# Kernel optimization log

Hardware: AMD Instinct MI355X
Metric: run time of the kernel (lower is better)

## Reference

```python
import jax, jax.numpy as jnp
import numpy as np

B, T, D, H, K = 128, 64, 2048, 512, 512
WINDOWS = [2, 3, 4]
ROUT = 2 * H            # bidirectional GRU output dim = 1024
FIN = ROUT + len(WINDOWS) * K + 2048 + 1024  # 5632 ('full' concat)
FOUT = 2048
BN_EPS = 1e-5


def setup_inputs() -> dict:
    key = jax.random.key(0)
    ks = jax.random.split(key, 32)
    s = 0.02
    inp = {
        "videos": jax.random.normal(ks[0], (B, T, D), jnp.float32),
        "motions": jax.random.normal(ks[1], (B, 1024), jnp.float32),
        "videos_origin": jax.random.normal(ks[2], (B, 2048), jnp.float32),
        "lengths": jax.random.randint(ks[3], (B,), 1, T + 1, jnp.int32),
        # GRU params (PyTorch layout: gates ordered r,z,n stacked on dim 0)
        "Wih_f": jax.random.normal(ks[4], (3 * H, D), jnp.float32) * s,
        "Whh_f": jax.random.normal(ks[5], (3 * H, H), jnp.float32) * s,
        "bih_f": jnp.zeros((3 * H,), jnp.float32),
        "bhh_f": jnp.zeros((3 * H,), jnp.float32),
        "Wih_b": jax.random.normal(ks[6], (3 * H, D), jnp.float32) * s,
        "Whh_b": jax.random.normal(ks[7], (3 * H, H), jnp.float32) * s,
        "bih_b": jnp.zeros((3 * H,), jnp.float32),
        "bhh_b": jnp.zeros((3 * H,), jnp.float32),
        # FC + BatchNorm1d (eval-mode) of MFC
        "fc_w": jax.random.normal(ks[8], (FOUT, FIN), jnp.float32) * (np.sqrt(6.0) / np.sqrt(FIN + FOUT)),
        "fc_b": jnp.zeros((FOUT,), jnp.float32),
        "bn_gamma": jnp.ones((FOUT,), jnp.float32),
        "bn_beta": jnp.zeros((FOUT,), jnp.float32),
        "bn_mean": jnp.zeros((FOUT,), jnp.float32),
        "bn_var": jnp.ones((FOUT,), jnp.float32),
    }
    for i, ws in enumerate(WINDOWS):
        inp[f"conv_w{ws}"] = jax.random.normal(ks[10 + 2 * i], (K, 1, ws, ROUT), jnp.float32) * s
        inp[f"conv_b{ws}"] = jnp.zeros((K,), jnp.float32)
    # mask consistent with lengths: mask[b,t] = t < lengths[b]
    inp["videos_mask"] = (jnp.arange(T)[None, :] < inp["lengths"][:, None]).astype(jnp.float32)
    return inp


def _gru_dir(x, Wih, Whh, bih, bhh, reverse):
    # x: [B,T,D] -> outputs [B,T,H]; torch GRU cell with r,z,n gate order
    xg = jnp.einsum("btd,gd->btg", x, Wih) + bih  # [B,T,3H] precomputed input gates

    def step(h, xg_t):
        hg = h @ Whh.T + bhh
        xr, xz, xn = jnp.split(xg_t, 3, axis=-1)
        hr, hz, hn = jnp.split(hg, 3, axis=-1)
        r = jax.nn.sigmoid(xr + hr)
        z = jax.nn.sigmoid(xz + hz)
        n = jnp.tanh(xn + r * hn)
        h_new = (1.0 - z) * n + z * h
        return h_new, h_new

    h0 = jnp.zeros((x.shape[0], Whh.shape[1]), x.dtype)
    _, hs = jax.lax.scan(step, h0, jnp.swapaxes(xg, 0, 1), reverse=reverse)
    return jnp.swapaxes(hs, 0, 1)


def _conv_branch(x4, w, b, ws):
    # x4: [B,1,T,ROUT], w: [K,1,ws,ROUT]; torch padding=(ws-1, 0)
    y = jax.lax.conv_general_dilated(
        x4, w, (1, 1), [(ws - 1, ws - 1), (0, 0)],
        dimension_numbers=("NCHW", "OIHW", "NCHW"))  # [B,K,T+ws-1,1]
    y = jax.nn.relu(y + b[None, :, None, None])
    return jnp.max(y, axis=(2, 3))  # max_pool1d over full time -> [B,K]


def _forward(videos, motions, videos_origin, lengths, videos_mask,
             Wih_f, Whh_f, bih_f, bhh_f, Wih_b, Whh_b, bih_b, bhh_b,
             conv_w2, conv_b2, conv_w3, conv_b3, conv_w4, conv_b4,
             fc_w, fc_b, bn_gamma, bn_beta, bn_mean, bn_var):
    fwd = _gru_dir(videos, Wih_f, Whh_f, bih_f, bhh_f, reverse=False)
    bwd = _gru_dir(videos, Wih_b, Whh_b, bih_b, bhh_b, reverse=True)
    gru_init_out = jnp.concatenate([fwd, bwd], axis=-1)  # [B,T,2H]

    # masked mean over valid frames (vectorized version of the batch for-loop)
    denom = lengths.astype(gru_init_out.dtype)[:, None]
    gru_out = jnp.sum(gru_init_out * videos_mask[:, :, None], axis=1) / denom  # [B,2H]

    masked = gru_init_out * videos_mask[:, :, None]
    x4 = masked[:, None, :, :]  # [B,1,T,2H]
    con_out = jnp.concatenate([
        _conv_branch(x4, conv_w2, conv_b2, 2),
        _conv_branch(x4, conv_w3, conv_b3, 3),
        _conv_branch(x4, conv_w4, conv_b4, 4),
    ], axis=1)  # [B,3K]

    # concate == 'full' (dropout is identity in eval)
    features = jnp.concatenate([gru_out, con_out, videos_origin, motions], axis=1)
    features = features @ fc_w.T + fc_b
    # BatchNorm1d, eval mode with running stats
    features = bn_gamma * (features - bn_mean) * jax.lax.rsqrt(bn_var + BN_EPS) + bn_beta
    # l2norm over dim 1
    features = features / jnp.sqrt(jnp.sum(features * features, axis=1, keepdims=True))
    return features


def reference(videos, motions, videos_origin, lengths, videos_mask,
              Wih_f, Whh_f, bih_f, bhh_f, Wih_b, Whh_b, bih_b, bhh_b,
              conv_w2, conv_b2, conv_w3, conv_b3, conv_w4, conv_b4,
              fc_w, fc_b, bn_gamma, bn_beta, bn_mean, bn_var):
    return _forward(videos, motions, videos_origin, lengths, videos_mask,
                    Wih_f, Whh_f, bih_f, bhh_f, Wih_b, Whh_b, bih_b, bhh_b,
                    conv_w2, conv_b2, conv_w3, conv_b3, conv_w4, conv_b4,
                    fc_w, fc_b, bn_gamma, bn_beta, bn_mean, bn_var)
```

## Files before the change

kernel.cpp:

```cpp
#include <hip/hip_runtime.h>
#include <hip/hip_bf16.h>
#include <stdint.h>

typedef __attribute__((ext_vector_type(8))) short short8;
typedef __attribute__((ext_vector_type(4))) float floatx4;
typedef __attribute__((ext_vector_type(4))) unsigned int u32x4;
typedef unsigned short u16;
typedef unsigned int u32;
typedef unsigned long long u64;

static __device__ __forceinline__ u16 f2bf(float f) {
  union { float f; u32 u; } v; v.f = f;
  return (u16)((v.u + 0x7fffu + ((v.u >> 16) & 1u)) >> 16);
}
static __device__ __forceinline__ float bf2f(u16 h) {
  union { u32 u; float f; } v; v.u = ((u32)h) << 16; return v.f;
}
static __device__ __forceinline__ u64 pack4(float a, float b, float c, float d) {
  return (u64)f2bf(a) | ((u64)f2bf(b) << 16) | ((u64)f2bf(c) << 32) | ((u64)f2bf(d) << 48);
}

__global__ __launch_bounds__(256) void k_fused_cvt(
    const float* __restrict__ videos, const float* __restrict__ Wih_f,
    const float* __restrict__ Wih_b, const float* __restrict__ Whh_f,
    const float* __restrict__ Whh_b, const float* __restrict__ fc_w,
    const float* __restrict__ w2, const float* __restrict__ w3,
    const float* __restrict__ w4, const float* __restrict__ vo,
    const float* __restrict__ mo, const float* __restrict__ bih_f,
    const float* __restrict__ bih_b, const float* __restrict__ fcb,
    const float* __restrict__ gam, const float* __restrict__ bet,
    const float* __restrict__ mu, const float* __restrict__ var,
    u16* __restrict__ vid, u16* __restrict__ wih, u16* __restrict__ whh,
    u16* __restrict__ fcw, u16* __restrict__ wc, u16* __restrict__ feat,
    float* __restrict__ bihcat, float* __restrict__ bns, float* __restrict__ bnt)
{
  const int O1 = 4194304;
  const int O2 = O1 + 786432;
  const int O3 = O2 + 786432;
  const int O4 = O3 + 196608;
  const int O5 = O4 + 196608;
  const int O6 = O5 + 2883584;
  const int O7 = O6 + 1179648;
  const int O8 = O7 + 65536;
  const int O9 = O8 + 32768;
  const int NQ = O9 + 1280;
  for (int q = blockIdx.x * 256 + threadIdx.x; q < NQ; q += gridDim.x * 256) {
    if (q < O1) {
      float4 v = ((const float4*)videos)[q];
      ((u64*)vid)[q] = pack4(v.x, v.y, v.z, v.w);
    } else if (q < O2) {
      int r = q - O1; float4 v = ((const float4*)Wih_f)[r];
      ((u64*)wih)[r] = pack4(v.x, v.y, v.z, v.w);
    } else if (q < O3) {
      int r = q - O2; float4 v = ((const float4*)Wih_b)[r];
      ((u64*)wih)[r + 786432] = pack4(v.x, v.y, v.z, v.w);
    } else if (q < O4) {
      int r = q - O3; float4 v = ((const float4*)Whh_f)[r];
      ((u64*)whh)[r] = pack4(v.x, v.y, v.z, v.w);
    } else if (q < O5) {
      int r = q - O4; float4 v = ((const float4*)Whh_b)[r];
      ((u64*)whh)[r + 196608] = pack4(v.x, v.y, v.z, v.w);
    } else if (q < O6) {
      int r = q - O5; float4 v = ((const float4*)fc_w)[r];
      ((u64*)fcw)[r] = pack4(v.x, v.y, v.z, v.w);
    } else if (q < O7) {
      int r = q - O6;
      int e = r << 2;
      int row = e >> 10, col = e & 1023;
      const float* src;
      if (row < 1024)      { int j = row >> 9, k = row & 511;                 src = w2 + (k * 2 + j) * 1024; }
      else if (row < 2560) { int m = row - 1024; int j = m >> 9, k = m & 511; src = w3 + (k * 3 + j) * 1024; }
      else                 { int m = row - 2560; int j = m >> 9, k = m & 511; src = w4 + (k * 4 + j) * 1024; }
      float4 v = *(const float4*)(src + col);
      ((u64*)wc)[r] = pack4(v.x, v.y, v.z, v.w);
    } else if (q < O8) {
      int r = q - O7; int b = r >> 9, c = (r & 511) * 4;
      float4 v = *(const float4*)&vo[(long)b * 2048 + c];
      *(u64*)&feat[(long)b * 5632 + 2560 + c] = pack4(v.x, v.y, v.z, v.w);
    } else if (q < O9) {
      int r = q - O8; int b = r >> 8, c = (r & 255) * 4;
      float4 v = *(const float4*)&mo[(long)b * 1024 + c];
      *(u64*)&feat[(long)b * 5632 + 4608 + c] = pack4(v.x, v.y, v.z, v.w);
    } else {
      int r = q - O9;
      if (r < 768) {
        int i = r * 4;
        const float* s = (i < 1536) ? (bih_f + i) : (bih_b + (i - 1536));
        *(float4*)&bihcat[i] = *(const float4*)s;
      } else {
        int i = (r - 768) * 4;
#pragma unroll
        for (int j = 0; j < 4; ++j) {
          int idx = i + j;
          float sc = gam[idx] * rsqrtf(var[idx] + 1e-5f);
          bns[idx] = sc;
          bnt[idx] = sc * (fcb[idx] - mu[idx]) + bet[idx];
        }
      }
    }
  }
}

static __device__ __forceinline__ void gload_lds16(const u16* g, u16* l) {
  __builtin_amdgcn_global_load_lds((const __attribute__((address_space(1))) u32*)(const void*)g,
                                   (__attribute__((address_space(3))) u32*)(void*)l, 16, 0, 0);
}

__global__ __launch_bounds__(256) void gemm_bt(
    const u16* __restrict__ A, const u16* __restrict__ Bm,
    float* __restrict__ C, u16* __restrict__ C16, int M, int N, int K, int kn,
    const float* __restrict__ scale, const float* __restrict__ shift)
{
  __shared__ u16 As[128 * 32];
  __shared__ u16 Bs[128 * 32];
  int tid = threadIdx.x, lane = tid & 63, wid = tid >> 6;
  int nwg = gridDim.x * gridDim.y;
  int lin = blockIdx.y * gridDim.x + blockIdx.x;
  int q8 = nwg >> 3;
  int swz = (lin & 7) * q8 + (lin >> 3);
  int m0 = (swz / gridDim.x) * 128, n0 = (swz % gridDim.x) * 128;
  int kt0 = blockIdx.z * kn;
  int wr = wid >> 1, wc = wid & 1;
  int r16 = lane & 15, kq = lane >> 4;
  const floatx4 z4 = {0.f, 0.f, 0.f, 0.f};
  floatx4 acc[4][4];
#pragma unroll
  for (int i = 0; i < 4; ++i)
#pragma unroll
    for (int j = 0; j < 4; ++j) acc[i][j] = z4;
  for (int kt = kt0; kt < kt0 + kn; ++kt) {
    __syncthreads();
#pragma unroll
    for (int inst = 0; inst < 2; ++inst) {
      int g = inst * 256 + tid;
      int row = g >> 2, cb = g & 3;
      const u16* ga = A + (long)(m0 + row) * K + kt * 32 + cb * 8;
      const u16* gb = Bm + (long)(n0 + row) * K + kt * 32 + cb * 8;
      gload_lds16(ga, &As[(inst * 256 + wid * 64) * 8]);
      gload_lds16(gb, &Bs[(inst * 256 + wid * 64) * 8]);
    }
    __syncthreads();
    short8 af[4], bf[4];
#pragma unroll
    for (int mt = 0; mt < 4; ++mt) af[mt] = *(const short8*)&As[(wr * 64 + mt * 16 + r16) * 32 + kq * 8];
#pragma unroll
    for (int nt = 0; nt < 4; ++nt) bf[nt] = *(const short8*)&Bs[(wc * 64 + nt * 16 + r16) * 32 + kq * 8];
#pragma unroll
    for (int mt = 0; mt < 4; ++mt)
#pragma unroll
      for (int nt = 0; nt < 4; ++nt)
        acc[mt][nt] = __builtin_amdgcn_mfma_f32_16x16x32_bf16(af[mt], bf[nt], acc[mt][nt], 0, 0, 0);
  }
  float* Cp = C + (long)blockIdx.z * M * N;
#pragma unroll
  for (int nt = 0; nt < 4; ++nt) {
    int col = n0 + wc * 64 + nt * 16 + r16;
    float sc = scale ? scale[col] : 1.f;
    float sh = shift ? shift[col] : 0.f;
#pragma unroll
    for (int mt = 0; mt < 4; ++mt)
#pragma unroll
      for (int q = 0; q < 4; ++q) {
        int row = m0 + wr * 64 + mt * 16 + kq * 4 + q;
        float v = acc[mt][nt][q] * sc + sh;
        if (C16) C16[(long)row * N + col] = f2bf(v);
        else     Cp[(long)row * N + col] = v;
      }
  }
}

__global__ __launch_bounds__(512) void gru_rec(
    const float* __restrict__ xg,
    const u16* __restrict__ whhb,
    const float* __restrict__ bhh_f, const float* __restrict__ bhh_b,
    u16* __restrict__ hbuf,
    u16* __restrict__ maskb,
    u16* __restrict__ feat,
    const int* __restrict__ lengths,
    int* __restrict__ flg)
{
  __shared__ float part[2][4][3][256];
  __shared__ u16 hstage[8192];
  int tid = threadIdx.x, lane = tid & 63, wid = tid >> 6;
  int bid = blockIdx.x;
  int dir = bid >> 6, rem = bid & 63, bt = rem >> 3, is = rem & 7;
  int ih = wid & 3, ks = wid >> 2;
  int gbase = (dir * 8 + bt) * 32;
  int r16 = lane & 15, kq = lane >> 4;
  int iglob = is * 64 + ih * 16 + r16;
  int i0 = is * 64 + ih * 16 + kq * 4;
  int batch = bt * 16 + r16;
  int pollidx = (gbase + (lane & 31)) * 16;
  int pubidx = (gbase + is * 4 + ih) * 16;
  const float* bhh = dir ? bhh_b : bhh_f;
  const floatx4 z4 = {0.f, 0.f, 0.f, 0.f};
  int len = lengths[batch];

  short8 wfrag[3][8];
#pragma unroll
  for (int g = 0; g < 3; ++g) {
    const u16* wrow = whhb + (long)(dir * 1536 + g * 512 + iglob) * 512;
#pragma unroll
    for (int kk = 0; kk < 8; ++kk)
      wfrag[g][kk] = *(const short8*)&wrow[(ks * 8 + kk) * 32 + kq * 8];
  }
  float4 bh4[3];
#pragma unroll
  for (int g = 0; g < 3; ++g) bh4[g] = *(const float4*)&bhh[g * 512 + i0];
  float4 hprev = {0.f, 0.f, 0.f, 0.f};
  float4 msum = {0.f, 0.f, 0.f, 0.f};

  float4 px[3];
  if (ks == 0) {
    int ts0 = dir ? 63 : 0;
    long xb = (long)(batch * 64 + ts0) * 3072 + dir * 1536 + i0;
#pragma unroll
    for (int g = 0; g < 3; ++g) px[g] = *(const float4*)&xg[xb + g * 512];
  }

  int so0 = wid * 2048 + lane * 16;
  int so1 = so0 + 1024;
  char* sl0 = (char*)hstage + (so0 ^ (((so0 >> 10) & 7) << 4));
  char* sl1 = (char*)hstage + (so1 ^ (((so1 >> 10) & 7) << 4));
  int rb = r16 * 1024 + ks * 512 + kq * 16;
  int rsw = (r16 & 7) << 4;

  for (int t = 0; t < 64; ++t) {
    if (t > 0) {
      if (wid == 0) {
        while (true) {
          int v;
          asm volatile("global_load_dword %0, %1, off sc0 sc1\n\ts_waitcnt vmcnt(0)"
                       : "=v"(v) : "v"(&flg[pollidx]) : "memory");
          if (__all(v >= t)) break;
          __builtin_amdgcn_s_sleep(1);
        }
      }
      asm volatile("s_barrier" ::: "memory");
    }
    int par = t & 1;
    const char* hsrc = (const char*)(hbuf + (long)((par * 2 + dir) * 128 + bt * 16) * 512);
    u32x4 qa, qb;
    asm volatile(
      "global_load_dwordx4 %0, %2, off sc0 sc1\n\t"
      "global_load_dwordx4 %1, %3, off sc0 sc1"
      : "=&v"(qa), "=&v"(qb)
      : "v"(hsrc + so0), "v"(hsrc + so1)
      : "memory");
    asm volatile("s_waitcnt vmcnt(0)" ::: "memory");
    *(u32x4*)sl0 = qa;
    *(u32x4*)sl1 = qb;
    float4 pxn[3];
    if (ks == 0 && t < 63) {
      int ts1 = dir ? (62 - t) : (t + 1);
      long xb = (long)(batch * 64 + ts1) * 3072 + dir * 1536 + i0;
#pragma unroll
      for (int g = 0; g < 3; ++g) pxn[g] = *(const float4*)&xg[xb + g * 512];
    }
    asm volatile("s_waitcnt lgkmcnt(0)\n\ts_barrier" ::: "memory");
    floatx4 acc[3];
#pragma unroll
    for (int g = 0; g < 3; ++g) acc[g] = z4;
#pragma unroll
    for (int kk = 0; kk < 8; ++kk) {
      short8 hv = *(const short8*)((const char*)hstage + ((rb + kk * 64) ^ rsw));
#pragma unroll
      for (int g = 0; g < 3; ++g)
        acc[g] = __builtin_amdgcn_mfma_f32_16x16x32_bf16(wfrag[g][kk], hv, acc[g], 0, 0, 0);
    }
    if (ks == 1) {
#pragma unroll
      for (int g = 0; g < 3; ++g) *(floatx4*)&part[par][ih][g][lane * 4] = acc[g];
    }
    asm volatile("s_waitcnt lgkmcnt(0)\n\ts_barrier" ::: "memory");
    if (ks == 0) {
      int tsrc = dir ? (63 - t) : t;
#pragma unroll
      for (int g = 0; g < 3; ++g) acc[g] += *(const floatx4*)&part[par][ih][g][lane * 4];
      float4 hn4;
#pragma unroll
      for (int q = 0; q < 4; ++q) {
        float rr = acc[0][q] + ((const float*)&bh4[0])[q] + ((const float*)&px[0])[q];
        float zz = acc[1][q] + ((const float*)&bh4[1])[q] + ((const float*)&px[1])[q];
        float r = 1.f / (1.f + __expf(-rr));
        float z = 1.f / (1.f + __expf(-zz));
        float n = tanhf(((const float*)&px[2])[q] + r * (acc[2][q] + ((const float*)&bh4[2])[q]));
        ((float*)&hn4)[q] = (1.f - z) * n + z * ((const float*)&hprev)[q];
      }
      hprev = hn4;
      u16* hdst = hbuf + (long)(((par ^ 1) * 2 + dir) * 128 + bt * 16) * 512;
      u64 hval = pack4(hn4.x, hn4.y, hn4.z, hn4.w);
      asm volatile("global_store_dwordx2 %0, %1, off sc0 sc1"
                   :: "v"((u64*)&hdst[r16 * 512 + i0]), "v"(hval) : "memory");
      if (t < 63) {
        asm volatile("s_waitcnt vmcnt(0)" ::: "memory");
        if (lane == 0) {
          int tv = t + 1;
          asm volatile("global_store_dword %0, %1, off sc0 sc1"
                       :: "v"(&flg[pubidx]), "v"(tv) : "memory");
        }
      }
      bool mv = tsrc < len;
      *(u64*)&maskb[(long)(batch * 64 + tsrc) * 1024 + dir * 512 + i0] = mv ? hval : 0ull;
      if (mv) {
        msum.x += hn4.x; msum.y += hn4.y; msum.z += hn4.z; msum.w += hn4.w;
      }
      px[0] = pxn[0]; px[1] = pxn[1]; px[2] = pxn[2];
    }
  }
  if (ks == 0) {
    float inv = 1.0f / (float)len;
    *(u64*)&feat[(long)batch * 5632 + dir * 512 + i0] =
        pack4(msum.x * inv, msum.y * inv, msum.z * inv, msum.w * inv);
  }
}

__global__ __launch_bounds__(256) void k_conv_finish(
    const u16* __restrict__ z, const float* __restrict__ cb2,
    const float* __restrict__ cb3, const float* __restrict__ cb4,
    u16* __restrict__ feat)
{
  int b = blockIdx.x, wsi = blockIdx.y, k2 = threadIdx.x * 2;
  int ws = wsi + 2;
  int base = (wsi == 0) ? 0 : (wsi == 1 ? 1024 : 2560);
  const float* cb = (wsi == 0) ? cb2 : (wsi == 1 ? cb3 : cb4);
  float bias0 = cb[k2], bias1 = cb[k2 + 1];
  float m0 = 0.f, m1 = 0.f;
  for (int p = 0; p < 64 + ws - 1; ++p) {
    float a0 = bias0, a1 = bias1;
    for (int j = 0; j < ws; ++j) {
      int t = p - (ws - 1) + j;
      if (t >= 0 && t < 64) {
        u32 v = *(const u32*)&z[(long)(b * 64 + t) * 4608 + base + j * 512 + k2];
        a0 += bf2f((u16)v);
        a1 += bf2f((u16)(v >> 16));
      }
    }
    m0 = fmaxf(m0, a0);
    m1 = fmaxf(m1, a1);
  }
  *(u32*)&feat[(long)b * 5632 + 1024 + wsi * 512 + k2] = (u32)f2bf(m0) | ((u32)f2bf(m1) << 16);
}

__global__ __launch_bounds__(256) void k_l2norm(const float* __restrict__ p,
    const float* __restrict__ bns, const float* __restrict__ bnt, float* __restrict__ out)
{
  __shared__ float red[4];
  int b = blockIdx.x, tid = threadIdx.x;
  float v[8]; float s = 0.f;
#pragma unroll
  for (int j = 0; j < 8; ++j) {
    int i = j * 256 + tid;
    long o = (long)b * 2048 + i;
    float a = 0.f;
#pragma unroll
    for (int zz = 0; zz < 8; ++zz) a += p[o + (long)zz * 262144];
    a = a * bns[i] + bnt[i];
    v[j] = a; s += a * a;
  }
#pragma unroll
  for (int o = 32; o > 0; o >>= 1) s += __shfl_down(s, o);
  if ((tid & 63) == 0) red[tid >> 6] = s;
  __syncthreads();
  float rn = rsqrtf(red[0] + red[1] + red[2] + red[3]);
#pragma unroll
  for (int j = 0; j < 8; ++j)
    out[(long)b * 2048 + j * 256 + tid] = v[j] * rn;
}

extern "C" void kernel_launch(void* const* d_in, const int* in_sizes, int n_in,
                              void* d_out, int out_size, void* d_ws, size_t ws_size,
                              hipStream_t stream)
{
  (void)in_sizes; (void)n_in; (void)out_size; (void)ws_size;
  const float* videos       = (const float*)d_in[0];
  const float* motions      = (const float*)d_in[1];
  const float* videos_origin= (const float*)d_in[2];
  const int*   lengths      = (const int*)d_in[3];
  const float* Wih_f = (const float*)d_in[4];
  const float* Whh_f = (const float*)d_in[5];
  const float* bih_f = (const float*)d_in[6];
  const float* bhh_f = (const float*)d_in[7];
  const float* Wih_b = (const float*)d_in[8];
  const float* Whh_b = (const float*)d_in[9];
  const float* bih_b = (const float*)d_in[10];
  const float* bhh_b = (const float*)d_in[11];
  const float* fc_w  = (const float*)d_in[12];
  const float* fc_b  = (const float*)d_in[13];
  const float* bn_gamma = (const float*)d_in[14];
  const float* bn_beta  = (const float*)d_in[15];
  const float* bn_mean  = (const float*)d_in[16];
  const float* bn_var   = (const float*)d_in[17];
  const float* conv_w2 = (const float*)d_in[18];
  const float* conv_b2 = (const float*)d_in[19];
  const float* conv_w3 = (const float*)d_in[20];
  const float* conv_b3 = (const float*)d_in[21];
  const float* conv_w4 = (const float*)d_in[22];
  const float* conv_b4 = (const float*)d_in[23];
  float* out = (float*)d_out;
  char* w = (char*)d_ws;

  const size_t XG    = 0;
  const size_t HS    = 100663296;
  const size_t VID   = 134217728;
  const size_t MASKB = 167772160;
  const size_t WIH   = 184549376;
  const size_t WHH   = 197132288;
  const size_t WC    = 200278016;
  const size_t FCW   = 209715200;
  const size_t FEAT  = 232783872;
  const size_t BIH   = 235274240;
  const size_t BNS   = 235286528;
  const size_t BNT   = 235294720;
  const size_t HB    = 235302912;
  const size_t FLG   = HB + 524288;
  (void)HS;

  float* xg   = (float*)(w + XG);
  u16*   zb16 = (u16*)(w + XG);
  u16* vid    = (u16*)(w + VID);
  u16* maskb  = (u16*)(w + MASKB);
  float* fcp  = (float*)(w + MASKB);
  u16* wih    = (u16*)(w + WIH);
  u16* whh    = (u16*)(w + WHH);
  u16* wc_    = (u16*)(w + WC);
  u16* fcw    = (u16*)(w + FCW);
  u16* feat   = (u16*)(w + FEAT);
  float* bih  = (float*)(w + BIH);
  float* bns  = (float*)(w + BNS);
  float* bnt  = (float*)(w + BNT);
  u16* hb     = (u16*)(w + HB);
  int* flg    = (int*)(w + FLG);

  hipMemsetAsync(w + HB, 0, 524288 + 32768, stream);

  k_fused_cvt<<<4096, 256, 0, stream>>>(
      videos, Wih_f, Wih_b, Whh_f, Whh_b, fc_w, conv_w2, conv_w3, conv_w4,
      videos_origin, motions, bih_f, bih_b, fc_b, bn_gamma, bn_beta, bn_mean, bn_var,
      vid, wih, whh, fcw, wc_, feat, bih, bns, bnt);

  gemm_bt<<<dim3(24, 64), 256, 0, stream>>>(vid, wih, xg, nullptr, 8192, 3072, 2048, 64, nullptr, bih);

  {
    const float* xg_c = xg; const u16* whh_c = whh;
    u16* hb_c = hb; u16* mb_c = maskb; u16* ft_c = feat;
    const int* len_c = lengths; int* flg_c = flg;
    const float* bf_c = bhh_f; const float* bb_c = bhh_b;
    void* args[] = { (void*)&xg_c, (void*)&whh_c, (void*)&bf_c, (void*)&bb_c,
                     (void*)&hb_c, (void*)&mb_c, (void*)&ft_c, (void*)&len_c, (void*)&flg_c };
    hipLaunchCooperativeKernel(reinterpret_cast<void*>(gru_rec), dim3(128), dim3(512), args, 0, stream);
  }

  gemm_bt<<<dim3(36, 64), 256, 0, stream>>>(maskb, wc_, nullptr, zb16, 8192, 4608, 1024, 32, nullptr, nullptr);
  k_conv_finish<<<dim3(128, 3), 256, 0, stream>>>(zb16, conv_b2, conv_b3, conv_b4, feat);
  gemm_bt<<<dim3(16, 1, 8), 256, 0, stream>>>(feat, fcw, fcp, nullptr, 128, 2048, 5632, 22, nullptr, nullptr);
  k_l2norm<<<128, 256, 0, stream>>>(fcp, bns, bnt, out);
}
```

Measured before the change: 641.6 us.

## Add 256x256-tile pipelined GEMM kernel for input-gate and conv GEMMs

Adds a new 512-thread GEMM kernel that uses 256x256 output tiles with 64-wide K tiles, double-buffered LDS loaded through global_load_lds, an XOR-swizzled LDS layout, and MFMA clusters interleaved with the staging of the next tile's halves under raised wave priority. The GRU input-gate GEMM and the conv-window GEMM switch from the 128x128 gemm_bt to this kernel. The aim is more operand reuse per LDS load and better overlap of global loads with MFMA work on these large GEMMs. In exchange it uses 128KB of LDS and many accumulators per wave, which limits occupancy, and its wrap-around prefetch indexing is intricate.

```diff
diff --git a/kernel.cpp b/kernel.cpp
--- a/kernel.cpp
+++ b/kernel.cpp
@@ -106,6 +106,154 @@
                                    (__attribute__((address_space(3))) u32*)(void*)l, 16, 0, 0);
 }
 
+static __device__ __forceinline__ void stage_half_256(
+    const u16* __restrict__ Mat, long K, int rowbase, int ktile, u16* lregion,
+    int tid, int wid)
+{
+  int srow = tid >> 3;
+  int sce = (((tid >> 3) ^ tid) & 7) * 8;
+  const u16* g0 = Mat + (long)(rowbase + srow) * K + ktile * 64 + sce;
+  const u16* g1 = Mat + (long)(rowbase + 64 + srow) * K + ktile * 64 + sce;
+  gload_lds16(g0, lregion + wid * 512);
+  gload_lds16(g1, lregion + 4096 + wid * 512);
+}
+
+__global__ __launch_bounds__(512) void gemm256(
+    const u16* __restrict__ A, const u16* __restrict__ Bm,
+    float* __restrict__ C, u16* __restrict__ C16, int M, int N, int K, int NT,
+    const float* __restrict__ shift)
+{
+  __shared__ u16 lds[65536];
+  int tid = threadIdx.x, lane = tid & 63, wid = tid >> 6;
+  int r16 = lane & 15, kq = lane >> 4;
+  int wr = wid >> 2, wc = wid & 3;
+  int nwg = gridDim.x * gridDim.y;
+  int lin = blockIdx.y * gridDim.x + blockIdx.x;
+  int q8 = nwg >> 3;
+  int swz = (lin & 7) * q8 + (lin >> 3);
+  int m0 = (swz / gridDim.x) * 256, n0 = (swz % gridDim.x) * 256;
+
+  int fxor = (r16 & 7) << 4;
+  int c0 = (kq * 16) ^ fxor;
+  int c1 = c0 ^ 64;
+  int brow0 = (wc & 1) * 64;
+  const char* ldsc = (const char*)lds;
+
+  const floatx4 z4 = {0.f, 0.f, 0.f, 0.f};
+  floatx4 acc[8][4];
+#pragma unroll
+  for (int i = 0; i < 8; ++i)
+#pragma unroll
+    for (int j = 0; j < 4; ++j) acc[i][j] = z4;
+
+  stage_half_256(Bm, K, n0,       0, lds,                 tid, wid);
+  stage_half_256(Bm, K, n0 + 128, 0, lds + 8192,          tid, wid);
+  stage_half_256(A,  K, m0,       0, lds + 16384,         tid, wid);
+  stage_half_256(A,  K, m0 + 128, 0, lds + 24576,         tid, wid);
+  stage_half_256(Bm, K, n0,       1, lds + 32768,         tid, wid);
+  stage_half_256(Bm, K, n0 + 128, 1, lds + 32768 + 8192,  tid, wid);
+  stage_half_256(A,  K, m0,       1, lds + 32768 + 16384, tid, wid);
+  stage_half_256(A,  K, m0 + 128, 1, lds + 32768 + 24576, tid, wid);
+  asm volatile("s_waitcnt vmcnt(8)" ::: "memory");
+  asm volatile("s_barrier" ::: "memory");
+
+#define MFMA_CLUSTER(q)                                                        \
+  asm volatile("s_waitcnt lgkmcnt(0)" ::: "memory");                           \
+  __builtin_amdgcn_sched_barrier(0);                                           \
+  __builtin_amdgcn_s_setprio(1);                                               \
+  _Pragma("unroll")                                                            \
+  for (int s = 0; s < 2; ++s)                                                  \
+    _Pragma("unroll")                                                          \
+    for (int e = 0; e < 2; ++e)                                                \
+      _Pragma("unroll")                                                        \
+      for (int j = 0; j < 4; ++j)                                              \
+        acc[(q)*2 + e][j] = __builtin_amdgcn_mfma_f32_16x16x32_bf16(           \
+            af[e][s], bf[j][s], acc[(q)*2 + e][j], 0, 0, 0);                   \
+  __builtin_amdgcn_s_setprio(0);
+
+  for (int T = 0; T < NT; ++T) {
+    int P = T & 1;
+    int Tn1 = (T + 1 < NT) ? T + 1 : 0;
+    int Tn2 = (T + 2 < NT) ? T + 2 : T + 2 - NT;
+    const char* bbase = ldsc + P * 65536 + (wc >> 1) * 16384;
+    const char* abase = ldsc + P * 65536 + 32768 + wr * 16384;
+    short8 bf[4][2];
+    {
+#pragma unroll
+      for (int j = 0; j < 4; ++j) {
+        bf[j][0] = *(const short8*)(bbase + (brow0 + j * 16 + r16) * 128 + c0);
+        bf[j][1] = *(const short8*)(bbase + (brow0 + j * 16 + r16) * 128 + c1);
+      }
+      short8 af[2][2];
+#pragma unroll
+      for (int e = 0; e < 2; ++e) {
+        af[e][0] = *(const short8*)(abase + (e * 16 + r16) * 128 + c0);
+        af[e][1] = *(const short8*)(abase + (e * 16 + r16) * 128 + c1);
+      }
+      stage_half_256(A, K, m0, Tn1, lds + (Tn1 & 1) * 32768 + 16384, tid, wid);
+      asm volatile("s_barrier" ::: "memory");
+      MFMA_CLUSTER(0)
+      asm volatile("s_barrier" ::: "memory");
+    }
+    {
+      short8 af[2][2];
+#pragma unroll
+      for (int e = 0; e < 2; ++e) {
+        af[e][0] = *(const short8*)(abase + ((2 + e) * 16 + r16) * 128 + c0);
+        af[e][1] = *(const short8*)(abase + ((2 + e) * 16 + r16) * 128 + c1);
+      }
+      stage_half_256(A, K, m0 + 128, Tn1, lds + (Tn1 & 1) * 32768 + 24576, tid, wid);
+      asm volatile("s_barrier" ::: "memory");
+      MFMA_CLUSTER(1)
+      asm volatile("s_barrier" ::: "memory");
+    }
+    {
+      short8 af[2][2];
+#pragma unroll
+      for (int e = 0; e < 2; ++e) {
+        af[e][0] = *(const short8*)(abase + ((4 + e) * 16 + r16) * 128 + c0);
+        af[e][1] = *(const short8*)(abase + ((4 + e) * 16 + r16) * 128 + c1);
+      }
+      stage_half_256(Bm, K, n0, Tn2, lds + P * 32768, tid, wid);
+      asm volatile("s_barrier" ::: "memory");
+      MFMA_CLUSTER(2)
+      asm volatile("s_barrier" ::: "memory");
+    }
+    {
+      short8 af[2][2];
+#pragma unroll
+      for (int e = 0; e < 2; ++e) {
+        af[e][0] = *(const short8*)(abase + ((6 + e) * 16 + r16) * 128 + c0);
+        af[e][1] = *(const short8*)(abase + ((6 + e) * 16 + r16) * 128 + c1);
+      }
+      stage_half_256(Bm, K, n0 + 128, Tn2, lds + P * 32768 + 8192, tid, wid);
+      asm volatile("s_barrier" ::: "memory");
+      MFMA_CLUSTER(3)
+      asm volatile("s_waitcnt vmcnt(4)" ::: "memory");
+      asm volatile("s_barrier" ::: "memory");
+    }
+  }
+#undef MFMA_CLUSTER
+
+#pragma unroll
+  for (int mf = 0; mf < 8; ++mf)
+#pragma unroll
+    for (int j = 0; j < 4; ++j) {
+      int col = n0 + wc * 64 + j * 16 + r16;
+      int row = m0 + wr * 128 + mf * 16 + kq * 4;
+      if (C16) {
+#pragma unroll
+        for (int qq = 0; qq < 4; ++qq)
+          C16[(long)(row + qq) * N + col] = f2bf(acc[mf][j][qq]);
+      } else {
+        float sh = shift ? shift[col] : 0.f;
+#pragma unroll
+        for (int qq = 0; qq < 4; ++qq)
+          C[(long)(row + qq) * N + col] = acc[mf][j][qq] + sh;
+      }
+    }
+}
+
 __global__ __launch_bounds__(256) void gemm_bt(
     const u16* __restrict__ A, const u16* __restrict__ Bm,
     float* __restrict__ C, u16* __restrict__ C16, int M, int N, int K, int kn,
@@ -401,7 +549,6 @@
   char* w = (char*)d_ws;
 
   const size_t XG    = 0;
-  const size_t HS    = 100663296;
   const size_t VID   = 134217728;
   const size_t MASKB = 167772160;
   const size_t WIH   = 184549376;
@@ -414,7 +561,6 @@
   const size_t BNT   = 235294720;
   const size_t HB    = 235302912;
   const size_t FLG   = HB + 524288;
-  (void)HS;
 
   float* xg   = (float*)(w + XG);
   u16*   zb16 = (u16*)(w + XG);
@@ -439,7 +585,7 @@
       videos_origin, motions, bih_f, bih_b, fc_b, bn_gamma, bn_beta, bn_mean, bn_var,
       vid, wih, whh, fcw, wc_, feat, bih, bns, bnt);
 
-  gemm_bt<<<dim3(24, 64), 256, 0, stream>>>(vid, wih, xg, nullptr, 8192, 3072, 2048, 64, nullptr, bih);
+  gemm256<<<dim3(12, 32), 512, 0, stream>>>(vid, wih, xg, nullptr, 8192, 3072, 2048, 32, bih);
 
   {
     const float* xg_c = xg; const u16* whh_c = whh;
@@ -451,7 +597,7 @@
     hipLaunchCooperativeKernel(reinterpret_cast<void*>(gru_rec), dim3(128), dim3(512), args, 0, stream);
   }
 
-  gemm_bt<<<dim3(36, 64), 256, 0, stream>>>(maskb, wc_, nullptr, zb16, 8192, 4608, 1024, 32, nullptr, nullptr);
+  gemm256<<<dim3(18, 32), 512, 0, stream>>>(maskb, wc_, nullptr, zb16, 8192, 4608, 1024, 16, nullptr);
   k_conv_finish<<<dim3(128, 3), 256, 0, stream>>>(zb16, conv_b2, conv_b3, conv_b4, feat);
   gemm_bt<<<dim3(16, 1, 8), 256, 0, stream>>>(feat, fcw, fcp, nullptr, 128, 2048, 5632, 22, nullptr, nullptr);
   k_l2norm<<<128, 256, 0, stream>>>(fcp, bns, bnt, out);
```

Measured after the change: 608.7 us. 1.05x faster.
